# Optimization experiments

Hardware: AMD Instinct MI355X
Metric: run time of the kernel (lower is better)

## Reference

```python
import jax, jax.numpy as jnp
import numpy as np

B, N, C, CD, R = 8, 16384, 32, 256, 32


def setup_inputs() -> dict:
    key = jax.random.key(0)
    ks = jax.random.split(key, 12)
    f32 = jnp.float32
    p = lambda k, shape, s=0.05: jax.random.normal(k, shape, f32) * s
    return {
        "features": jax.random.normal(ks[0], (B, C, N), f32),
        "coords": jax.random.normal(ks[1], (B, 3, N), f32),
        "condition": jax.random.normal(ks[2], (B, CD), f32),
        "conv1_w": p(ks[3], (C, C, 3, 3, 3)), "conv1_b": jnp.zeros((C,), f32),
        "gn1_g": jnp.ones((C,), f32), "gn1_b": jnp.zeros((C,), f32),
        "mod1_w": p(ks[4], (2 * C, CD)),
        "mod1_b": jnp.concatenate([jnp.ones((C,)), jnp.zeros((C,))]).astype(f32),
        "conv2_w": p(ks[5], (C, C, 3, 3, 3)), "conv2_b": jnp.zeros((C,), f32),
        "gn2_g": jnp.ones((C,), f32), "gn2_b": jnp.zeros((C,), f32),
        "mod2_w": p(ks[6], (2 * C, CD)),
        "mod2_b": jnp.concatenate([jnp.ones((C,)), jnp.zeros((C,))]).astype(f32),
        "se_w1": p(ks[7], (C // 8, C)), "se_w2": p(ks[8], (C, C // 8)),
        "pc_w": p(ks[9], (C, C)), "pc_b": jnp.zeros((C,), f32),
        "gnp_g": jnp.ones((C,), f32), "gnp_b": jnp.zeros((C,), f32),
        "modp_w": p(ks[10], (2 * C, CD)),
        "modp_b": jnp.concatenate([jnp.ones((C,)), jnp.zeros((C,))]).astype(f32),
    }


def group_norm(x, g, b, G=8, eps=1e-5):
    shape = x.shape
    xg = x.reshape(shape[0], G, -1)
    m = xg.mean(-1, keepdims=True)
    v = xg.var(-1, keepdims=True)
    xn = ((xg - m) * jax.lax.rsqrt(v + eps)).reshape(shape)
    bshape = (1, shape[1]) + (1,) * (x.ndim - 2)
    return xn * g.reshape(bshape) + b.reshape(bshape)


def adagn(x, c, g, b, mw, mb):
    # GroupNorm then scale/shift from SiLU(c) @ Linear
    x = group_norm(x, g, b)
    m = jax.nn.silu(c) @ mw.T + mb  # (B, 2C)
    scale, shift = jnp.split(m, 2, axis=1)
    bshape = (x.shape[0], x.shape[1]) + (1,) * (x.ndim - 2)
    return x * scale.reshape(bshape) + shift.reshape(bshape)


def voxelize(features, coords, r):
    # scatter-average point features into r^3 grid; coords detached as in torch
    coords = jax.lax.stop_gradient(coords)
    nc = coords - coords.mean(2, keepdims=True)
    denom = jnp.max(jnp.linalg.norm(nc, axis=1, keepdims=True), axis=2, keepdims=True) * 2.0
    nc = nc / denom + 0.5
    nc = jnp.clip(nc * r, 0, r - 1)  # (B,3,N) continuous in [0, r-1]
    vc = jnp.round(nc).astype(jnp.int32)
    idx = (vc[:, 0] * r + vc[:, 1]) * r + vc[:, 2]  # (B,N) flat voxel ids

    def per_batch(f, i):
        s = jax.ops.segment_sum(f.T, i, num_segments=r ** 3)  # (V, D)
        cnt = jax.ops.segment_sum(jnp.ones(i.shape, f.dtype), i, num_segments=r ** 3)
        return (s / jnp.maximum(cnt, 1.0)[:, None]).T.reshape(f.shape[0], r, r, r)

    vox = jax.vmap(per_batch)(features, idx)  # (B, D, r, r, r)
    return vox, nc


def devoxelize(vox, coords, r):
    # trilinear gather of voxel features back to points
    Bv, D = vox.shape[:2]
    flat = vox.reshape(Bv, D, r * r * r)
    lo = jnp.floor(coords)
    frac = coords - lo
    lo = lo.astype(jnp.int32)
    hi = jnp.minimum(lo + 1, r - 1)
    gather = jax.vmap(lambda f, i: f[:, i])  # per-batch (D,V)[:, (N,)] -> (D,N)
    out = jnp.zeros((Bv, D, coords.shape[2]), vox.dtype)
    for dx in (0, 1):
        ix = hi[:, 0] if dx else lo[:, 0]
        wx = frac[:, 0] if dx else 1.0 - frac[:, 0]
        for dy in (0, 1):
            iy = hi[:, 1] if dy else lo[:, 1]
            wy = frac[:, 1] if dy else 1.0 - frac[:, 1]
            for dz in (0, 1):
                iz = hi[:, 2] if dz else lo[:, 2]
                wz = frac[:, 2] if dz else 1.0 - frac[:, 2]
                idx = (ix * r + iy) * r + iz
                out = out + gather(flat, idx) * (wx * wy * wz)[:, None, :]
    return out


def conv3d(x, w, b):
    y = jax.lax.conv_general_dilated(x, w, (1, 1, 1), 'SAME',
                                     dimension_numbers=('NCDHW', 'OIDHW', 'NCDHW'))
    return y + b[None, :, None, None, None]


def reference(features, coords, condition, conv1_w, conv1_b, gn1_g, gn1_b, mod1_w,
              mod1_b, conv2_w, conv2_b, gn2_g, gn2_b, mod2_w, mod2_b, se_w1, se_w2,
              pc_w, pc_b, gnp_g, gnp_b, modp_w, modp_b):
    vox, nc = voxelize(features, coords, R)
    v = conv3d(vox, conv1_w, conv1_b)
    v = jax.nn.silu(adagn(v, condition, gn1_g, gn1_b, mod1_w, mod1_b))
    v = conv3d(v, conv2_w, conv2_b)
    v = adagn(v, condition, gn2_g, gn2_b, mod2_w, mod2_b)
    # SE3d squeeze-excite
    s = jax.nn.sigmoid(jax.nn.relu(v.mean((2, 3, 4)) @ se_w1.T) @ se_w2.T)
    v = v * s[:, :, None, None, None]
    vfeat = devoxelize(v, nc, R)  # (B, C, N)
    # point branch: 1x1 conv + AdaGN + SiLU
    px = jnp.einsum('bdn,od->bon', features, pc_w) + pc_b[None, :, None]
    px = jax.nn.silu(adagn(px, condition, gnp_g, gnp_b, modp_w, modp_b))
    return vfeat + px
```

## Files before the change

kernel.cpp:

```cpp
#include <hip/hip_runtime.h>
#include <math.h>

#define DEV_INLINE __device__ __forceinline__

namespace {

typedef unsigned short u16;
typedef unsigned int u32;
typedef __attribute__((ext_vector_type(8))) short short8v;
typedef __attribute__((ext_vector_type(16))) float f32x16;

constexpr int Bn = 8, Cn = 32, Nn = 16384, Rn = 32, Vn = Rn * Rn * Rn;

DEV_INLINE float siluf(float x) { return x / (1.0f + __expf(-x)); }
DEV_INLINE float bf2f(u16 u) { union { u32 i; float f; } x; x.i = (u32)u << 16; return x.f; }
DEV_INLINE u16 f2bf(float f) {
  union { float f; u32 i; } x; x.f = f;
  return (u16)((x.i + 0x7FFFu + ((x.i >> 16) & 1u)) >> 16);
}
DEV_INLINE u32 pack2(float a, float b) { return (u32)f2bf(a) | ((u32)f2bf(b) << 16); }
DEV_INLINE void unpack8(uint4 u, float* f) {
  f[0] = bf2f(u.x & 0xffff); f[1] = bf2f(u.x >> 16);
  f[2] = bf2f(u.y & 0xffff); f[3] = bf2f(u.y >> 16);
  f[4] = bf2f(u.z & 0xffff); f[5] = bf2f(u.z >> 16);
  f[6] = bf2f(u.w & 0xffff); f[7] = bf2f(u.w >> 16);
}

__global__ void k_cpart1(const float* __restrict__ coords, float* __restrict__ csum) {
  int blk = blockIdx.x;
  int b = blk >> 3, s = blk & 7;
  int t = threadIdx.x;
  const float* cb = coords + (size_t)b * 3 * Nn;
  int n0 = s * 2048;
  float sx = 0.f, sy = 0.f, sz = 0.f;
  for (int n = n0 + t; n < n0 + 2048; n += 256) {
    sx += cb[n]; sy += cb[Nn + n]; sz += cb[2 * Nn + n];
  }
  #pragma unroll
  for (int m = 1; m <= 32; m <<= 1) {
    sx += __shfl_xor(sx, m); sy += __shfl_xor(sy, m); sz += __shfl_xor(sz, m);
  }
  __shared__ float rs[3][4];
  if ((t & 63) == 0) { rs[0][t >> 6] = sx; rs[1][t >> 6] = sy; rs[2][t >> 6] = sz; }
  __syncthreads();
  if (t < 3) atomicAdd(&csum[b * 4 + t], rs[t][0] + rs[t][1] + rs[t][2] + rs[t][3]);
}

__global__ void k_cpart2(const float* __restrict__ coords, const float* __restrict__ csum,
                         int* __restrict__ cmax) {
  int blk = blockIdx.x;
  int b = blk >> 3, s = blk & 7;
  int t = threadIdx.x;
  const float* cb = coords + (size_t)b * 3 * Nn;
  const float invn = 1.0f / (float)Nn;
  float mx = csum[b * 4] * invn, my = csum[b * 4 + 1] * invn, mz = csum[b * 4 + 2] * invn;
  int n0 = s * 2048;
  float mq = 0.f;
  for (int n = n0 + t; n < n0 + 2048; n += 256) {
    float x = cb[n] - mx, y = cb[Nn + n] - my, z = cb[2 * Nn + n] - mz;
    mq = fmaxf(mq, x * x + y * y + z * z);
  }
  #pragma unroll
  for (int m = 1; m <= 32; m <<= 1) mq = fmaxf(mq, __shfl_xor(mq, m));
  __shared__ float rm[4];
  if ((t & 63) == 0) rm[t >> 6] = mq;
  __syncthreads();
  if (t == 0) {
    float v = fmaxf(fmaxf(rm[0], rm[1]), fmaxf(rm[2], rm[3]));
    atomicMax(cmax + b, __float_as_int(v));
  }
}

__global__ void k_cfinal(const float* __restrict__ coords, const float* __restrict__ csum,
                         const int* __restrict__ cmax, float* __restrict__ nc,
                         int* __restrict__ vidx, int* __restrict__ hist) {
  int i = blockIdx.x * 256 + threadIdx.x;
  int b = i >> 14, n = i & (Nn - 1);
  const float* cb = coords + (size_t)b * 3 * Nn;
  const float invn = 1.0f / (float)Nn;
  float mx = csum[b * 4] * invn, my = csum[b * 4 + 1] * invn, mz = csum[b * 4 + 2] * invn;
  float inv = 1.0f / (2.0f * sqrtf(__int_as_float(cmax[b])));
  float x = (cb[n] - mx) * inv + 0.5f;
  float y = (cb[Nn + n] - my) * inv + 0.5f;
  float z = (cb[2 * Nn + n] - mz) * inv + 0.5f;
  x = fminf(fmaxf(x * (float)Rn, 0.f), (float)(Rn - 1));
  y = fminf(fmaxf(y * (float)Rn, 0.f), (float)(Rn - 1));
  z = fminf(fmaxf(z * (float)Rn, 0.f), (float)(Rn - 1));
  float* ncb = nc + (size_t)b * 3 * Nn;
  ncb[n] = x; ncb[Nn + n] = y; ncb[2 * Nn + n] = z;
  int vx = (int)rintf(x), vy = (int)rintf(y), vz = (int)rintf(z);
  int v = (vx * Rn + vy) * Rn + vz;
  vidx[i] = v;
  atomicAdd(&hist[b * Vn + v], 1);
}

__global__ __launch_bounds__(256, 2) void k_pxlin(
    const float* __restrict__ feat, const float* __restrict__ w,
    const float* __restrict__ bias, float* __restrict__ featT,
    u16* __restrict__ pxb) {
  __shared__ float lw[1024];
  __shared__ float lb[32];
  __shared__ float lbuf[256 * 33];
  int t = threadIdx.x;
  for (int i = t; i < 1024; i += 256) lw[i] = w[i];
  if (t < 32) lb[t] = bias[t];
  int blk = blockIdx.x;
  int b = blk >> 6, tile = blk & 63;
  int n0 = tile * 256, n = n0 + t;
  float fr[32];
  const float* fb = feat + (size_t)b * 32 * Nn + n;
  #pragma unroll
  for (int ci = 0; ci < 32; ++ci) {
    fr[ci] = fb[(size_t)ci * Nn];
    lbuf[t * 33 + ci] = fr[ci];
  }
  __syncthreads();
  float* ftb = featT + ((size_t)b * Nn + n0) * 32;
  #pragma unroll
  for (int j = 0; j < 32; ++j) {
    int idx = j * 256 + t;
    ftb[idx] = lbuf[(idx >> 5) * 33 + (idx & 31)];
  }
  __syncthreads();
  u32* lbu = reinterpret_cast<u32*>(lbuf);
  #pragma unroll
  for (int p2 = 0; p2 < 16; ++p2) {
    int co0 = p2 * 2;
    float a0 = lb[co0], a1 = lb[co0 + 1];
    #pragma unroll
    for (int ci = 0; ci < 32; ++ci) {
      a0 += lw[co0 * 32 + ci] * fr[ci];
      a1 += lw[(co0 + 1) * 32 + ci] * fr[ci];
    }
    lbu[t * 17 + p2] = pack2(a0, a1);
  }
  __syncthreads();
  u32* pxu = reinterpret_cast<u32*>(pxb) + ((size_t)b * Nn + n0) * 16;
  #pragma unroll
  for (int j = 0; j < 16; ++j) {
    int idx = j * 256 + t;
    pxu[idx] = lbu[(idx >> 4) * 17 + (idx & 15)];
  }
}

__global__ void k_scan1(const int* __restrict__ hist, int* __restrict__ offs,
                        int* __restrict__ bsum) {
  __shared__ int sd[256];
  int t = threadIdx.x, blk = blockIdx.x;
  int4 h = reinterpret_cast<const int4*>(hist)[blk * 256 + t];
  int s = h.x + h.y + h.z + h.w;
  sd[t] = s; __syncthreads();
  for (int off = 1; off < 256; off <<= 1) {
    int add = (t >= off) ? sd[t - off] : 0;
    __syncthreads();
    sd[t] += add;
    __syncthreads();
  }
  int excl = sd[t] - s;
  int4 o;
  o.x = excl; o.y = excl + h.x; o.z = o.y + h.y; o.w = o.z + h.z;
  reinterpret_cast<int4*>(offs)[blk * 256 + t] = o;
  if (t == 0) bsum[blk] = sd[255];
}

__global__ void k_scan2(const int* __restrict__ bsum, int* __restrict__ bbase) {
  __shared__ int sd[256];
  int t = threadIdx.x;
  int s = bsum[t];
  sd[t] = s; __syncthreads();
  for (int off = 1; off < 256; off <<= 1) {
    int add = (t >= off) ? sd[t - off] : 0;
    __syncthreads();
    sd[t] += add;
    __syncthreads();
  }
  bbase[t] = sd[t] - s;
}

__global__ void k_sortidx(const int* __restrict__ vidx, int* __restrict__ offs,
                          const int* __restrict__ bbase, int* __restrict__ pidx) {
  int i = blockIdx.x * 256 + threadIdx.x;
  int b = i >> 14, n = i & (Nn - 1);
  int g = b * Vn + vidx[i];
  int p = atomicAdd(&offs[g], 1) + bbase[g >> 10];
  pidx[p] = n;
}

__global__ void k_voxavg(const int* __restrict__ hist, const int* __restrict__ offs,
                         const int* __restrict__ bbase, const int* __restrict__ pidx,
                         const float* __restrict__ featT, uint2* __restrict__ vox0) {
  int t = threadIdx.x;
  int wv = blockIdx.x * 4 + (t >> 6);
  int lane = t & 63;
  int c4 = lane & 7, j = lane >> 3;
  int b = wv >> 15;
  int cnt = hist[wv];
  float ax = 0.f, ay = 0.f, az = 0.f, aw = 0.f;
  if (cnt > 0) {
    int end = offs[wv] + bbase[wv >> 10];
    int start = end - cnt;
    const float4* ft = reinterpret_cast<const float4*>(featT) + (size_t)b * Nn * 8;
    for (int k = start + j; k < end; k += 8) {
      int n = pidx[k];
      float4 v = ft[n * 8 + c4];
      ax += v.x; ay += v.y; az += v.z; aw += v.w;
    }
    #pragma unroll
    for (int m = 8; m <= 32; m <<= 1) {
      ax += __shfl_xor(ax, m); ay += __shfl_xor(ay, m);
      az += __shfl_xor(az, m); aw += __shfl_xor(aw, m);
    }
    float invc = 1.0f / (float)cnt;
    ax *= invc; ay *= invc; az *= invc; aw *= invc;
  }
  if (j == 0) {
    uint2 o;
    o.x = pack2(ax, ay);
    o.y = pack2(az, aw);
    vox0[(size_t)wv * 8 + c4] = o;
  }
}

__global__ void k_twz(const float* __restrict__ w, u16* __restrict__ wt) {
  int i = blockIdx.x * 256 + threadIdx.x;
  if (i >= 27 * 32 * 32) return;
  int e = i & 7, l = (i >> 3) & 63, h = (i >> 9) & 1, k = i >> 10;
  int co = l & 31, ci = h * 16 + ((l >> 5) << 3) + e;
  wt[i] = f2bf(w[(co * 32 + ci) * 27 + k]);
}

__global__ void k_mods(const float* __restrict__ cond,
                       const float* __restrict__ w1, const float* __restrict__ b1,
                       const float* __restrict__ w2, const float* __restrict__ b2,
                       const float* __restrict__ wp, const float* __restrict__ bp,
                       float* __restrict__ m1, float* __restrict__ m2,
                       float* __restrict__ mp) {
  int blk = blockIdx.x;
  int mat = blk >> 3, b = blk & 7;
  int t = threadIdx.x;
  __shared__ float sc[256];
  sc[t] = siluf(cond[b * 256 + t]);
  __syncthreads();
  const float* w = (mat == 0) ? w1 : ((mat == 1) ? w2 : wp);
  const float* bb = (mat == 0) ? b1 : ((mat == 1) ? b2 : bp);
  float* dst = (mat == 0) ? m1 : ((mat == 1) ? m2 : mp);
  int wave = t >> 6, lane = t & 63;
  const float4* w4 = reinterpret_cast<const float4*>(w);
  float4 sv = reinterpret_cast<const float4*>(sc)[lane];
  #pragma unroll
  for (int i = 0; i < 16; ++i) {
    int oo = wave * 16 + i;
    float4 wv = w4[oo * 64 + lane];
    float p = wv.x * sv.x + wv.y * sv.y + wv.z * sv.z + wv.w * sv.w;
    #pragma unroll
    for (int m = 1; m <= 32; m <<= 1) p += __shfl_xor(p, m);
    if (lane == 0) dst[b * 64 + oo] = p + bb[oo];
  }
}

__global__ __launch_bounds__(512, 2) void k_conv(
    const u16* __restrict__ in, const u16* __restrict__ wt,
    const float* __restrict__ bias, u16* __restrict__ out,
    float* __restrict__ pstat) {
  __shared__ uint4 lds_w4[3456];
  __shared__ uint4 lds_x4[4096];
  int t = threadIdx.x;
  int blk = blockIdx.x;
  int yp = blk & 3, x = (blk >> 2) & 31, b = blk >> 7;
  int y0 = yp * 8;
  size_t bbase = (size_t)b * Vn;

  const uint4* gw = reinterpret_cast<const uint4*>(wt);
  for (int i = t; i < 3456; i += 512) lds_w4[i] = gw[i];

  for (int i = t; i < 4080; i += 512) {
    int col = i / 136, rem = i - col * 136;
    int c4 = rem / 34, r = rem - c4 * 34;
    int dxp = col / 10, yy = col - dxp * 10;
    int gx = x + dxp - 1, gy = y0 + yy - 1, z = r - 1;
    uint4 val = make_uint4(0u, 0u, 0u, 0u);
    if (gx >= 0 && gx < 32 && (unsigned)gy < 32u && (unsigned)z < 32u) {
      val = *reinterpret_cast<const uint4*>(
          in + (bbase + (size_t)((gx * 32 + gy) * 32 + z)) * 32 + c4 * 8);
    }
    lds_x4[i] = val;
  }
  __syncthreads();

  int w = t >> 6, lane = t & 63;
  int zc = lane & 31, hi = lane >> 5;
  int y = y0 + w;

  f32x16 acc;
  #pragma unroll
  for (int q = 0; q < 4; ++q) {
    float4 bq = *reinterpret_cast<const float4*>(bias + q * 8 + hi * 4);
    acc[q * 4 + 0] = bq.x; acc[q * 4 + 1] = bq.y;
    acc[q * 4 + 2] = bq.z; acc[q * 4 + 3] = bq.w;
  }

  const u16* lw = reinterpret_cast<const u16*>(lds_w4);
  const u16* lx = reinterpret_cast<const u16*>(lds_x4);

  #pragma unroll
  for (int dxp = 0; dxp < 3; ++dxp) {
    #pragma unroll
    for (int dyp = 0; dyp < 3; ++dyp) {
      int col = dxp * 10 + w + dyp;
      #pragma unroll
      for (int dzp = 0; dzp < 3; ++dzp) {
        int k = (dxp * 3 + dyp) * 3 + dzp;
        short8v a0 = *reinterpret_cast<const short8v*>(lw + ((k * 2 + 0) * 64 + lane) * 8);
        short8v a1 = *reinterpret_cast<const short8v*>(lw + ((k * 2 + 1) * 64 + lane) * 8);
        short8v b0 = *reinterpret_cast<const short8v*>(
            lx + ((col * 4 + hi) * 34 + zc + dzp) * 8);
        short8v b1 = *reinterpret_cast<const short8v*>(
            lx + ((col * 4 + 2 + hi) * 34 + zc + dzp) * 8);
        acc = __builtin_amdgcn_mfma_f32_32x32x16_bf16(a0, b0, acc, 0, 0, 0);
        acc = __builtin_amdgcn_mfma_f32_32x32x16_bf16(a1, b1, acc, 0, 0, 0);
      }
    }
  }

  size_t off = (bbase + (size_t)((x * 32 + y) * 32 + zc)) * 32;
  #pragma unroll
  for (int q = 0; q < 4; ++q) {
    uint2 o;
    o.x = pack2(acc[q * 4 + 0], acc[q * 4 + 1]);
    o.y = pack2(acc[q * 4 + 2], acc[q * 4 + 3]);
    *reinterpret_cast<uint2*>(out + off + q * 8 + hi * 4) = o;
  }

  float s16[16], q16[16];
  #pragma unroll
  for (int r = 0; r < 16; ++r) { s16[r] = acc[r]; q16[r] = acc[r] * acc[r]; }
  #pragma unroll
  for (int m = 1; m <= 16; m <<= 1) {
    #pragma unroll
    for (int r = 0; r < 16; ++r) {
      s16[r] += __shfl_xor(s16[r], m);
      q16[r] += __shfl_xor(q16[r], m);
    }
  }
  __syncthreads();
  float* sred = reinterpret_cast<float*>(lds_w4);
  if ((lane & 31) == 0) {
    #pragma unroll
    for (int r = 0; r < 16; ++r) {
      int co = (r & 3) + 8 * (r >> 2) + 4 * hi;
      sred[w * 64 + co] = s16[r];
      sred[512 + w * 64 + co] = q16[r];
    }
  }
  __syncthreads();
  if (t < 64) {
    int arr = t >> 5, c = t & 31;
    const float* bp_ = sred + arr * 512 + c;
    float v = bp_[0] + bp_[64] + bp_[128] + bp_[192] +
              bp_[256] + bp_[320] + bp_[384] + bp_[448];
    pstat[blk * 64 + arr * 32 + c] = v;
  }
}

__global__ void k_affsilu(uint4* __restrict__ x, const float* __restrict__ Ac,
                          const float* __restrict__ Bc) {
  int i = blockIdx.x * 256 + threadIdx.x;
  int c4 = i & 3, b = i >> 17;
  uint4 v = x[i];
  float f[8];
  unpack8(v, f);
  float4 A0 = reinterpret_cast<const float4*>(Ac)[b * 8 + c4 * 2];
  float4 A1 = reinterpret_cast<const float4*>(Ac)[b * 8 + c4 * 2 + 1];
  float4 B0 = reinterpret_cast<const float4*>(Bc)[b * 8 + c4 * 2];
  float4 B1 = reinterpret_cast<const float4*>(Bc)[b * 8 + c4 * 2 + 1];
  f[0] = siluf(f[0] * A0.x + B0.x); f[1] = siluf(f[1] * A0.y + B0.y);
  f[2] = siluf(f[2] * A0.z + B0.z); f[3] = siluf(f[3] * A0.w + B0.w);
  f[4] = siluf(f[4] * A1.x + B1.x); f[5] = siluf(f[5] * A1.y + B1.y);
  f[6] = siluf(f[6] * A1.z + B1.z); f[7] = siluf(f[7] * A1.w + B1.w);
  uint4 o;
  o.x = pack2(f[0], f[1]); o.y = pack2(f[2], f[3]);
  o.z = pack2(f[4], f[5]); o.w = pack2(f[6], f[7]);
  x[i] = o;
}

__global__ void k_statspx(const u16* __restrict__ x, float* __restrict__ psum,
                          float* __restrict__ psq, int segs) {
  int blk = blockIdx.x;
  int b = blk / segs;
  int t = threadIdx.x;
  int c8 = t & 3, vsub = t >> 2;
  float s[8], q[8];
  #pragma unroll
  for (int j = 0; j < 8; ++j) { s[j] = 0.f; q[j] = 0.f; }
  const uint4* xb = reinterpret_cast<const uint4*>(x) + (size_t)blk * 4096;
  for (int it = 0; it < 16; ++it) {
    int v = it * 64 + vsub;
    uint4 u = xb[v * 4 + c8];
    float f[8];
    unpack8(u, f);
    #pragma unroll
    for (int j = 0; j < 8; ++j) { s[j] += f[j]; q[j] += f[j] * f[j]; }
  }
  #pragma unroll
  for (int m = 4; m <= 32; m <<= 1) {
    #pragma unroll
    for (int j = 0; j < 8; ++j) {
      s[j] += __shfl_xor(s[j], m);
      q[j] += __shfl_xor(q[j], m);
    }
  }
  __shared__ float ls[2][4][4][8];
  int wv = t >> 6;
  if ((t & 63) < 4) {
    #pragma unroll
    for (int j = 0; j < 8; ++j) { ls[0][wv][c8][j] = s[j]; ls[1][wv][c8][j] = q[j]; }
  }
  __syncthreads();
  if (t < 64) {
    int arr = t >> 5, c = t & 31;
    float v = ls[arr][0][c >> 3][c & 7] + ls[arr][1][c >> 3][c & 7] +
              ls[arr][2][c >> 3][c & 7] + ls[arr][3][c >> 3][c & 7];
    atomicAdd((arr == 0 ? psum : psq) + b * 32 + c, v);
  }
}

__global__ void k_coef1(const float* __restrict__ pstat, const float* __restrict__ mod,
                        const float* __restrict__ g, const float* __restrict__ bgn,
                        float* __restrict__ A, float* __restrict__ Bc) {
  int t = threadIdx.x;
  int b = t >> 5, c = t & 31;
  float cs = 0.f, cq = 0.f;
  const float* p = pstat + (size_t)b * 128 * 64;
  for (int i = 0; i < 128; ++i) {
    cs += p[i * 64 + c];
    cq += p[i * 64 + 32 + c];
  }
  __shared__ float ls[256], lq[256];
  ls[t] = cs; lq[t] = cq;
  __syncthreads();
  int gb = t & ~3;
  float s4 = ls[gb] + ls[gb + 1] + ls[gb + 2] + ls[gb + 3];
  float q4 = lq[gb] + lq[gb + 1] + lq[gb + 2] + lq[gb + 3];
  const float cntf = 4.0f * (float)Vn;
  float mean = s4 / cntf;
  float var = q4 / cntf - mean * mean;
  float rstd = rsqrtf(var + 1e-5f);
  float scale = mod[b * 64 + c], shift = mod[b * 64 + 32 + c];
  A[t] = rstd * g[c] * scale;
  Bc[t] = (bgn[c] - mean * rstd * g[c]) * scale + shift;
}

__global__ void k_coef2(const float* __restrict__ pstat, const float* __restrict__ mod,
                        const float* __restrict__ g, const float* __restrict__ bgn,
                        const float* __restrict__ sw1, const float* __restrict__ sw2,
                        float* __restrict__ S, float* __restrict__ T) {
  __shared__ float zm[8][32];
  __shared__ float hh[8][4];
  __shared__ float ls[256], lq[256];
  int t = threadIdx.x;
  int b = t >> 5, c = t & 31;
  float cs = 0.f, cq = 0.f;
  const float* p = pstat + (size_t)b * 128 * 64;
  for (int i = 0; i < 128; ++i) {
    cs += p[i * 64 + c];
    cq += p[i * 64 + 32 + c];
  }
  ls[t] = cs; lq[t] = cq;
  __syncthreads();
  int gb = t & ~3;
  float s4 = ls[gb] + ls[gb + 1] + ls[gb + 2] + ls[gb + 3];
  float q4 = lq[gb] + lq[gb + 1] + lq[gb + 2] + lq[gb + 3];
  const float cntf = 4.0f * (float)Vn;
  float mean = s4 / cntf;
  float var = q4 / cntf - mean * mean;
  float rstd = rsqrtf(var + 1e-5f);
  float scale = mod[b * 64 + c], shift = mod[b * 64 + 32 + c];
  float A = rstd * g[c] * scale;
  float Bv = (bgn[c] - mean * rstd * g[c]) * scale + shift;
  float chmean = cs / (float)Vn;
  zm[b][c] = A * chmean + Bv;
  __syncthreads();
  if (t < 32) {
    int b2 = t >> 2, j = t & 3;
    float h = 0;
    for (int cc = 0; cc < 32; ++cc) h += sw1[j * 32 + cc] * zm[b2][cc];
    hh[b2][j] = fmaxf(h, 0.f);
  }
  __syncthreads();
  float sig = 0;
  for (int j = 0; j < 4; ++j) sig += sw2[c * 4 + j] * hh[b][j];
  sig = 1.0f / (1.0f + __expf(-sig));
  S[t] = A * sig;
  T[t] = Bv * sig;
}

__global__ void k_coefp(const float* __restrict__ psum, const float* __restrict__ psq,
                        const float* __restrict__ mod, const float* __restrict__ g,
                        const float* __restrict__ bgn, float* __restrict__ A,
                        float* __restrict__ Bc) {
  __shared__ float ls[256], lq[256];
  int t = threadIdx.x;
  int b = t >> 5, c = t & 31;
  ls[t] = psum[t]; lq[t] = psq[t];
  __syncthreads();
  int gb = t & ~3;
  float s4 = ls[gb] + ls[gb + 1] + ls[gb + 2] + ls[gb + 3];
  float q4 = lq[gb] + lq[gb + 1] + lq[gb + 2] + lq[gb + 3];
  const float cntf = 4.0f * (float)Nn;
  float m = s4 / cntf;
  float var = q4 / cntf - m * m;
  float r = rsqrtf(var + 1e-5f);
  float scale = mod[b * 64 + c], shift = mod[b * 64 + 32 + c];
  A[t] = r * g[c] * scale;
  Bc[t] = (bgn[c] - m * r * g[c]) * scale + shift;
}

__global__ void k_devoxfinal(const u16* __restrict__ vox, const float* __restrict__ nc,
                             const u16* __restrict__ pxb, const float* __restrict__ S,
                             const float* __restrict__ T, const float* __restrict__ Ap,
                             const float* __restrict__ Bp, float* __restrict__ out) {
  int i = blockIdx.x * 256 + threadIdx.x;
  int b = i >> 14, n = i & (Nn - 1);
  const float* ncb = nc + (size_t)b * 3 * Nn;
  float fx = ncb[n], fy = ncb[Nn + n], fz = ncb[2 * Nn + n];
  float lxf = floorf(fx), lyf = floorf(fy), lzf = floorf(fz);
  float wx1 = fx - lxf, wy1 = fy - lyf, wz1 = fz - lzf;
  int lx = (int)lxf, ly = (int)lyf, lz = (int)lzf;
  int hx = min(lx + 1, 31), hy = min(ly + 1, 31), hz = min(lz + 1, 31);
  float a[32];
  #pragma unroll
  for (int c = 0; c < 32; ++c) a[c] = 0.f;
  for (int corner = 0; corner < 8; ++corner) {
    int cx = (corner & 4) ? hx : lx;
    int cy = (corner & 2) ? hy : ly;
    int cz = (corner & 1) ? hz : lz;
    float ww = ((corner & 4) ? wx1 : 1.f - wx1) *
               ((corner & 2) ? wy1 : 1.f - wy1) *
               ((corner & 1) ? wz1 : 1.f - wz1);
    const uint4* p = reinterpret_cast<const uint4*>(
        vox + ((size_t)b * Vn + (size_t)((cx * 32 + cy) * 32 + cz)) * 32);
    #pragma unroll
    for (int qq = 0; qq < 4; ++qq) {
      float f[8];
      unpack8(p[qq], f);
      #pragma unroll
      for (int j = 0; j < 8; ++j) a[qq * 8 + j] += ww * f[j];
    }
  }
  const uint4* pp = reinterpret_cast<const uint4*>(pxb) + (size_t)i * 4;
  float* o = out + (size_t)b * 32 * Nn + n;
  #pragma unroll
  for (int qq = 0; qq < 4; ++qq) {
    float pf[8];
    unpack8(pp[qq], pf);
    #pragma unroll
    for (int j = 0; j < 8; ++j) {
      int c = qq * 8 + j;
      float y = pf[j] * Ap[b * 32 + c] + Bp[b * 32 + c];
      o[(size_t)c * Nn] = a[c] * S[b * 32 + c] + T[b * 32 + c] + siluf(y);
    }
  }
}

}

extern "C" void kernel_launch(void* const* d_in, const int* in_sizes, int n_in,
                              void* d_out, int out_size, void* d_ws, size_t ws_size,
                              hipStream_t stream) {
  (void)in_sizes; (void)n_in; (void)out_size; (void)ws_size;
  const float* features = (const float*)d_in[0];
  const float* coords = (const float*)d_in[1];
  const float* condition = (const float*)d_in[2];
  const float* conv1_w = (const float*)d_in[3];
  const float* conv1_b = (const float*)d_in[4];
  const float* gn1_g = (const float*)d_in[5];
  const float* gn1_b = (const float*)d_in[6];
  const float* mod1_w = (const float*)d_in[7];
  const float* mod1_b = (const float*)d_in[8];
  const float* conv2_w = (const float*)d_in[9];
  const float* conv2_b = (const float*)d_in[10];
  const float* gn2_g = (const float*)d_in[11];
  const float* gn2_b = (const float*)d_in[12];
  const float* mod2_w = (const float*)d_in[13];
  const float* mod2_b = (const float*)d_in[14];
  const float* se_w1 = (const float*)d_in[15];
  const float* se_w2 = (const float*)d_in[16];
  const float* pc_w = (const float*)d_in[17];
  const float* pc_b = (const float*)d_in[18];
  const float* gnp_g = (const float*)d_in[19];
  const float* gnp_b = (const float*)d_in[20];
  const float* modp_w = (const float*)d_in[21];
  const float* modp_b = (const float*)d_in[22];

  char* w = (char*)d_ws;
  float* featT = (float*)w;
  u16* vox1 = (u16*)w;
  w += 16777216;
  u16* vox2 = (u16*)w; w += 16777216;
  u16* vox0 = (u16*)w; w += 16777216;
  u16* pxb = (u16*)w;  w += 8388608;
  int* hist = (int*)w;  w += 1048576;
  float* psump = (float*)w; w += 1024;
  float* psqp = (float*)w;  w += 1024;
  float* csum = (float*)w;  w += 128;
  int* cmax = (int*)w;      w += 64;
  int* offs = (int*)w;  w += 1048576;
  int* bsum = (int*)w;  w += 1024;
  int* bbase = (int*)w; w += 1024;
  int* pidx = (int*)w;  w += 524288;
  float* ncb = (float*)w;   w += 1572864;
  int* vidx = (int*)w;      w += 524288;
  u16* wt1b = (u16*)w;      w += 55296;
  u16* wt2b = (u16*)w;      w += 55296;
  float* pstat1 = (float*)w; w += 262144;
  float* pstat2 = (float*)w; w += 262144;
  float* m1 = (float*)w;    w += 2048;
  float* m2 = (float*)w;    w += 2048;
  float* mp = (float*)w;    w += 2048;
  float* A1 = (float*)w;    w += 1024;
  float* B1 = (float*)w;    w += 1024;
  float* Sc = (float*)w;    w += 1024;
  float* Tc = (float*)w;    w += 1024;
  float* Ap = (float*)w;    w += 1024;
  float* Bp = (float*)w;    w += 1024;
  float* out = (float*)d_out;

  hipMemsetAsync(hist, 0, 1048576 + 1024 + 1024 + 128 + 64, stream);

  k_pxlin<<<Bn * 64, 256, 0, stream>>>(features, pc_w, pc_b, featT, pxb);
  k_cpart1<<<Bn * 8, 256, 0, stream>>>(coords, csum);
  k_twz<<<108, 256, 0, stream>>>(conv1_w, wt1b);
  k_twz<<<108, 256, 0, stream>>>(conv2_w, wt2b);
  k_mods<<<24, 256, 0, stream>>>(condition, mod1_w, mod1_b, mod2_w, mod2_b,
                                 modp_w, modp_b, m1, m2, mp);
  k_statspx<<<Bn * 16, 256, 0, stream>>>(pxb, psump, psqp, 16);
  k_coefp<<<1, 256, 0, stream>>>(psump, psqp, mp, gnp_g, gnp_b, Ap, Bp);
  k_cpart2<<<Bn * 8, 256, 0, stream>>>(coords, csum, cmax);
  k_cfinal<<<(Bn * Nn) / 256, 256, 0, stream>>>(coords, csum, cmax, ncb, vidx, hist);
  k_scan1<<<256, 256, 0, stream>>>(hist, offs, bsum);
  k_scan2<<<1, 256, 0, stream>>>(bsum, bbase);
  k_sortidx<<<(Bn * Nn) / 256, 256, 0, stream>>>(vidx, offs, bbase, pidx);
  k_voxavg<<<(Bn * Vn) / 4, 256, 0, stream>>>(hist, offs, bbase, pidx, featT,
                                              (uint2*)vox0);
  k_conv<<<1024, 512, 0, stream>>>(vox0, wt1b, conv1_b, vox1, pstat1);
  k_coef1<<<1, 256, 0, stream>>>(pstat1, m1, gn1_g, gn1_b, A1, B1);
  k_affsilu<<<4096, 256, 0, stream>>>((uint4*)vox1, A1, B1);
  k_conv<<<1024, 512, 0, stream>>>(vox1, wt2b, conv2_b, vox2, pstat2);
  k_coef2<<<1, 256, 0, stream>>>(pstat2, m2, gn2_g, gn2_b, se_w1, se_w2, Sc, Tc);
  k_devoxfinal<<<(Bn * Nn) / 256, 256, 0, stream>>>(vox2, ncb, pxb, Sc, Tc, Ap, Bp, out);
}
```

Baseline: 240.7 us.

## Fuse AdaGN+SiLU into conv2 halo load and read conv weights from global

Removes the standalone affine+SiLU pass over vox1 and applies it in conv2 while staging the input tile into LDS. Padding voxels stay zero, which matches SAME padding applied after the activation. Conv weights are no longer staged in LDS; each MFMA reads its A operand straight from global/L2, which halves LDS use and raises launch bounds to 4 blocks per SM. The costs are recomputing SiLU on halo voxels that neighbouring tiles overlap, and global-load latency inside the MFMA loop.

```diff
diff --git a/kernel.cpp b/kernel.cpp
--- a/kernel.cpp
+++ b/kernel.cpp
@@ -258,20 +258,18 @@
   }
 }
 
-__global__ __launch_bounds__(512, 2) void k_conv(
+template <bool AFF>
+__global__ __launch_bounds__(512, 4) void k_conv(
     const u16* __restrict__ in, const u16* __restrict__ wt,
-    const float* __restrict__ bias, u16* __restrict__ out,
+    const float* __restrict__ bias, const float* __restrict__ Ac,
+    const float* __restrict__ Bc, u16* __restrict__ out,
     float* __restrict__ pstat) {
-  __shared__ uint4 lds_w4[3456];
   __shared__ uint4 lds_x4[4096];
   int t = threadIdx.x;
   int blk = blockIdx.x;
   int yp = blk & 3, x = (blk >> 2) & 31, b = blk >> 7;
   int y0 = yp * 8;
   size_t bbase = (size_t)b * Vn;
-
-  const uint4* gw = reinterpret_cast<const uint4*>(wt);
-  for (int i = t; i < 3456; i += 512) lds_w4[i] = gw[i];
 
   for (int i = t; i < 4080; i += 512) {
     int col = i / 136, rem = i - col * 136;
@@ -282,6 +280,20 @@
     if (gx >= 0 && gx < 32 && (unsigned)gy < 32u && (unsigned)z < 32u) {
       val = *reinterpret_cast<const uint4*>(
           in + (bbase + (size_t)((gx * 32 + gy) * 32 + z)) * 32 + c4 * 8);
+      if (AFF) {
+        float f[8];
+        unpack8(val, f);
+        float4 A0 = reinterpret_cast<const float4*>(Ac)[b * 8 + c4 * 2];
+        float4 A1 = reinterpret_cast<const float4*>(Ac)[b * 8 + c4 * 2 + 1];
+        float4 B0 = reinterpret_cast<const float4*>(Bc)[b * 8 + c4 * 2];
+        float4 B1 = reinterpret_cast<const float4*>(Bc)[b * 8 + c4 * 2 + 1];
+        f[0] = siluf(f[0] * A0.x + B0.x); f[1] = siluf(f[1] * A0.y + B0.y);
+        f[2] = siluf(f[2] * A0.z + B0.z); f[3] = siluf(f[3] * A0.w + B0.w);
+        f[4] = siluf(f[4] * A1.x + B1.x); f[5] = siluf(f[5] * A1.y + B1.y);
+        f[6] = siluf(f[6] * A1.z + B1.z); f[7] = siluf(f[7] * A1.w + B1.w);
+        val.x = pack2(f[0], f[1]); val.y = pack2(f[2], f[3]);
+        val.z = pack2(f[4], f[5]); val.w = pack2(f[6], f[7]);
+      }
     }
     lds_x4[i] = val;
   }
@@ -299,8 +311,8 @@
     acc[q * 4 + 2] = bq.z; acc[q * 4 + 3] = bq.w;
   }
 
-  const u16* lw = reinterpret_cast<const u16*>(lds_w4);
   const u16* lx = reinterpret_cast<const u16*>(lds_x4);
+  const u16* gw = wt + lane * 8;
 
   #pragma unroll
   for (int dxp = 0; dxp < 3; ++dxp) {
@@ -310,8 +322,8 @@
       #pragma unroll
       for (int dzp = 0; dzp < 3; ++dzp) {
         int k = (dxp * 3 + dyp) * 3 + dzp;
-        short8v a0 = *reinterpret_cast<const short8v*>(lw + ((k * 2 + 0) * 64 + lane) * 8);
-        short8v a1 = *reinterpret_cast<const short8v*>(lw + ((k * 2 + 1) * 64 + lane) * 8);
+        short8v a0 = *reinterpret_cast<const short8v*>(gw + (k * 2 + 0) * 512);
+        short8v a1 = *reinterpret_cast<const short8v*>(gw + (k * 2 + 1) * 512);
         short8v b0 = *reinterpret_cast<const short8v*>(
             lx + ((col * 4 + hi) * 34 + zc + dzp) * 8);
         short8v b1 = *reinterpret_cast<const short8v*>(
@@ -343,7 +355,7 @@
     }
   }
   __syncthreads();
-  float* sred = reinterpret_cast<float*>(lds_w4);
+  float* sred = reinterpret_cast<float*>(lds_x4);
   if ((lane & 31) == 0) {
     #pragma unroll
     for (int r = 0; r < 16; ++r) {
@@ -360,27 +372,6 @@
               bp_[256] + bp_[320] + bp_[384] + bp_[448];
     pstat[blk * 64 + arr * 32 + c] = v;
   }
-}
-
-__global__ void k_affsilu(uint4* __restrict__ x, const float* __restrict__ Ac,
-                          const float* __restrict__ Bc) {
-  int i = blockIdx.x * 256 + threadIdx.x;
-  int c4 = i & 3, b = i >> 17;
-  uint4 v = x[i];
-  float f[8];
-  unpack8(v, f);
-  float4 A0 = reinterpret_cast<const float4*>(Ac)[b * 8 + c4 * 2];
-  float4 A1 = reinterpret_cast<const float4*>(Ac)[b * 8 + c4 * 2 + 1];
-  float4 B0 = reinterpret_cast<const float4*>(Bc)[b * 8 + c4 * 2];
-  float4 B1 = reinterpret_cast<const float4*>(Bc)[b * 8 + c4 * 2 + 1];
-  f[0] = siluf(f[0] * A0.x + B0.x); f[1] = siluf(f[1] * A0.y + B0.y);
-  f[2] = siluf(f[2] * A0.z + B0.z); f[3] = siluf(f[3] * A0.w + B0.w);
-  f[4] = siluf(f[4] * A1.x + B1.x); f[5] = siluf(f[5] * A1.y + B1.y);
-  f[6] = siluf(f[6] * A1.z + B1.z); f[7] = siluf(f[7] * A1.w + B1.w);
-  uint4 o;
-  o.x = pack2(f[0], f[1]); o.y = pack2(f[2], f[3]);
-  o.z = pack2(f[4], f[5]); o.w = pack2(f[6], f[7]);
-  x[i] = o;
 }
 
 __global__ void k_statspx(const u16* __restrict__ x, float* __restrict__ psum,
@@ -642,10 +633,10 @@
   k_sortidx<<<(Bn * Nn) / 256, 256, 0, stream>>>(vidx, offs, bbase, pidx);
   k_voxavg<<<(Bn * Vn) / 4, 256, 0, stream>>>(hist, offs, bbase, pidx, featT,
                                               (uint2*)vox0);
-  k_conv<<<1024, 512, 0, stream>>>(vox0, wt1b, conv1_b, vox1, pstat1);
+  k_conv<false><<<1024, 512, 0, stream>>>(vox0, wt1b, conv1_b, nullptr, nullptr,
+                                          vox1, pstat1);
   k_coef1<<<1, 256, 0, stream>>>(pstat1, m1, gn1_g, gn1_b, A1, B1);
-  k_affsilu<<<4096, 256, 0, stream>>>((uint4*)vox1, A1, B1);
-  k_conv<<<1024, 512, 0, stream>>>(vox1, wt2b, conv2_b, vox2, pstat2);
+  k_conv<true><<<1024, 512, 0, stream>>>(vox1, wt2b, conv2_b, A1, B1, vox2, pstat2);
   k_coef2<<<1, 256, 0, stream>>>(pstat2, m2, gn2_g, gn2_b, se_w1, se_w2, Sc, Tc);
   k_devoxfinal<<<(Bn * Nn) / 256, 256, 0, stream>>>(vox2, ncb, pxb, Sc, Tc, Ap, Bp, out);
 }
```

Measured after the change: 222.1 us. -7.7%, faster.
